# Kernel optimization log

Measured on AMD Instinct MI355X. Metric: run time of the kernel, lower is better.

Reference implementation:

```python
import jax, jax.numpy as jnp
import numpy as np

D = 1024
H = 16
HD = D // H
FF = 4096
B = 2
S = 2048


def _layer_norm(x, g, b, eps=1e-5):
    mu = jnp.mean(x, axis=-1, keepdims=True)
    var = jnp.mean(jnp.square(x - mu), axis=-1, keepdims=True)
    return (x - mu) * jax.lax.rsqrt(var + eps) * g + b


def setup_inputs() -> dict:
    key = jax.random.key(0)
    ks = jax.random.split(key, 16)
    s = 0.02
    return {
        "x": jax.random.normal(ks[0], (B, S, D), jnp.float32),
        "Wq": jax.random.normal(ks[1], (H, D, HD), jnp.float32) * s,
        "bq": jnp.zeros((H, HD), jnp.float32),
        "Wk": jax.random.normal(ks[2], (H, D, HD), jnp.float32) * s,
        "bk": jnp.zeros((H, HD), jnp.float32),
        "Wv": jax.random.normal(ks[3], (H, D, HD), jnp.float32) * s,
        "bv": jnp.zeros((H, HD), jnp.float32),
        "Wo": jax.random.normal(ks[4], (D, D), jnp.float32) * s,
        "bo": jnp.zeros((D,), jnp.float32),
        "W1": jax.random.normal(ks[5], (D, FF), jnp.float32) * s,
        "b1": jnp.zeros((FF,), jnp.float32),
        "W2": jax.random.normal(ks[6], (FF, D), jnp.float32) * s,
        "b2": jnp.zeros((D,), jnp.float32),
        "g1": jnp.ones((D,), jnp.float32),
        "be1": jnp.zeros((D,), jnp.float32),
        "g2": jnp.ones((D,), jnp.float32),
        "be2": jnp.zeros((D,), jnp.float32),
    }


def reference(x, Wq, bq, Wk, bk, Wv, bv, Wo, bo, W1, b1, W2, b2, g1, be1, g2, be2):
    b, s, d = x.shape
    # per-head projections (vectorized over heads)
    q = jnp.einsum("bsd,hde->bhse", x, Wq) + bq[None, :, None, :]
    k = jnp.einsum("bsd,hde->bhse", x, Wk) + bk[None, :, None, :]
    v = jnp.einsum("bsd,hde->bhse", x, Wv) + bv[None, :, None, :]
    # NOTE: source scales by 1/dim_k (not 1/sqrt(dim_k)) -- kept faithful
    scores = jnp.einsum("bhse,bhte->bhst", q, k) / jnp.asarray(HD, x.dtype)
    causal = jnp.tril(jnp.ones((s, s), bool))  # [S,S]
    scores = jnp.where(causal[None, None], scores, jnp.asarray(-jnp.inf, x.dtype))
    attn = jax.nn.softmax(scores, axis=-1)
    ctx = jnp.einsum("bhst,bhte->bhse", attn, v)  # [B,H,S,hd]
    ctx = jnp.transpose(ctx, (0, 2, 1, 3)).reshape(b, s, d)  # concat heads
    attn_out = ctx @ Wo + bo
    x = _layer_norm(x + attn_out, g1, be1)
    # feed-forward: linear -> exact GELU -> linear (dropout = eval identity)
    h = jax.nn.gelu(x @ W1 + b1, approximate=False)
    ff = h @ W2 + b2
    return _layer_norm(x + ff, g2, be2)
```

## Files before the change

kernel.cpp:

```cpp
#include <hip/hip_runtime.h>
#include <math.h>

constexpr int Dm  = 1024;
constexpr int Hh  = 16;
constexpr int HDm = 64;
constexpr int FFm = 4096;
constexpr int Bb  = 2;
constexpr int Sq  = 2048;
constexpr int Mm  = Bb * Sq;

typedef __attribute__((ext_vector_type(8))) short short8;
typedef __attribute__((ext_vector_type(4))) short short4v;
typedef __attribute__((ext_vector_type(4))) float f32x4;

#define AS1 __attribute__((address_space(1)))
#define AS3 __attribute__((address_space(3)))

constexpr float QSCALE = 0.022542110013890054f;

__device__ __forceinline__ unsigned short f2b(float f) {
    union { float f; unsigned u; } v; v.f = f;
    unsigned r = v.u + 0x7FFFu + ((v.u >> 16) & 1u);
    return (unsigned short)(r >> 16);
}

__device__ __forceinline__ float gelu_fast(float x) {
    float z = x * (2.302080918f + 0.102938049f * x * x);
    return x * __builtin_amdgcn_rcpf(1.0f + exp2f(-z));
}

__global__ __launch_bounds__(256) void convert_x(const float* __restrict__ x,
                                                 short* __restrict__ xb) {
    int i = blockIdx.x * 256 + threadIdx.x;
    float4 v = ((const float4*)x)[i];
    short4v o;
    o[0] = (short)f2b(v.x); o[1] = (short)f2b(v.y);
    o[2] = (short)f2b(v.z); o[3] = (short)f2b(v.w);
    ((short4v*)xb)[i] = o;
}

__global__ __launch_bounds__(256) void transpose_to_bf16(
    const float* __restrict__ src, short* __restrict__ dst, int R, int C) {
    __shared__ float t[64][65];
    const int c0 = blockIdx.x * 64, r0 = blockIdx.y * 64;
    const int lc = threadIdx.x & 63, lr4 = threadIdx.x >> 6;
    #pragma unroll
    for (int p = 0; p < 16; ++p) {
        int rr = p * 4 + lr4;
        t[rr][lc] = src[(size_t)(r0 + rr) * C + c0 + lc];
    }
    __syncthreads();
    #pragma unroll
    for (int p = 0; p < 16; ++p) {
        int rr = p * 4 + lr4;
        dst[(size_t)(c0 + rr) * R + r0 + lc] = (short)f2b(t[lc][rr]);
    }
}

__global__ __launch_bounds__(256) void build_wqkv(
    const float* __restrict__ Wq, const float* __restrict__ Wk,
    const float* __restrict__ Wv, short* __restrict__ dst) {
    const int kt = blockIdx.x, h = blockIdx.y, which = blockIdx.z;
    const float* W = ((which == 0) ? Wq : (which == 1) ? Wk : Wv) +
                     (size_t)h * Dm * HDm;
    __shared__ float t[64][65];
    const int lc = threadIdx.x & 63, lr4 = threadIdx.x >> 6;
    #pragma unroll
    for (int p = 0; p < 16; ++p) {
        int kr = p * 4 + lr4;
        t[kr][lc] = W[(size_t)(kt * 64 + kr) * HDm + lc];
    }
    __syncthreads();
    const int nbase = which * 1024 + h * 64;
    #pragma unroll
    for (int p = 0; p < 16; ++p) {
        int e = p * 4 + lr4;
        dst[(size_t)(nbase + e) * Dm + kt * 64 + lc] = (short)f2b(t[lc][e]);
    }
}

__global__ __launch_bounds__(256) void build_bqkv(
    const float* __restrict__ bq, const float* __restrict__ bk,
    const float* __restrict__ bv, float* __restrict__ bcat) {
    int n = blockIdx.x * 256 + threadIdx.x;
    const float* s = (n < 1024) ? bq : (n < 2048) ? bk : bv;
    bcat[n] = s[n & 1023];
}

template<int EPI>
__global__ __launch_bounds__(512, 2) void gemm256(
    const short* __restrict__ A, const short* __restrict__ Bt,
    const float* __restrict__ bias,
    short* __restrict__ outb,
    short* __restrict__ qo, short* __restrict__ ko, short* __restrict__ vo,
    int K, int N, int NMT)
{
    __shared__ __align__(16) char lds[131072];
    char* const ldsA = lds;
    char* const ldsB = lds + 65536;
    const int tid = threadIdx.x;
    const int l = tid & 63, wv = tid >> 6;
    const int wm = wv >> 2, wn = wv & 3;
    const int lr = l & 15, lg = l >> 4;
    const int bid = blockIdx.x;
    const int m0 = (bid % NMT) * 256;
    const int n0 = (bid / NMT) * 256;
    const size_t KB = (size_t)K * 2;
    const int NT = K >> 6;

    const char* pA[2][2];
    const char* pB[2][2];
    #pragma unroll
    for (int i = 0; i < 2; ++i) {
        int c = tid + 512 * i;
        int rh = c >> 3, j = c & 7;
        int sw = (j ^ (rh & 7)) << 4;
        #pragma unroll
        for (int h = 0; h < 2; ++h) {
            pA[h][i] = (const char*)A + (size_t)(m0 + h * 128 + rh) * KB + sw;
            pB[h][i] = (const char*)Bt + (size_t)(n0 + h * 128 + rh) * KB + sw;
        }
    }
    const int dbase = tid * 16;

    f32x4 acc[8][4];
    f32x4 z4 = {0.f, 0.f, 0.f, 0.f};
    #pragma unroll
    for (int i = 0; i < 8; ++i)
        #pragma unroll
        for (int j = 0; j < 4; ++j) acc[i][j] = z4;

#define STAGE_B(h, nb) do {                                                     \
    char* _b = ldsB + ((nb) * 2 + (h)) * 16384;                                 \
    __builtin_amdgcn_global_load_lds((const AS1 void*)pB[h][0],                 \
        (AS3 void*)(_b + dbase), 16, 0, 0);                                     \
    __builtin_amdgcn_global_load_lds((const AS1 void*)pB[h][1],                 \
        (AS3 void*)(_b + dbase + 8192), 16, 0, 0);                              \
    pB[h][0] += 128; pB[h][1] += 128; } while (0)
#define STAGE_A(h, nb) do {                                                     \
    char* _a = ldsA + ((nb) * 2 + (h)) * 16384;                                 \
    __builtin_amdgcn_global_load_lds((const AS1 void*)pA[h][0],                 \
        (AS3 void*)(_a + dbase), 16, 0, 0);                                     \
    __builtin_amdgcn_global_load_lds((const AS1 void*)pA[h][1],                 \
        (AS3 void*)(_a + dbase + 8192), 16, 0, 0);                              \
    pA[h][0] += 128; pA[h][1] += 128; } while (0)

    STAGE_B(0, 0); STAGE_B(1, 0); STAGE_A(0, 0); STAGE_A(1, 0);
    asm volatile("s_waitcnt vmcnt(2)" ::: "memory");
    __builtin_amdgcn_s_barrier();
    __builtin_amdgcn_sched_barrier(0);

    const int swk0 = ((0 + lg) ^ (lr & 7)) << 4;
    const int swk1 = ((4 + lg) ^ (lr & 7)) << 4;

    for (int kt = 0; kt < NT; ++kt) {
        const int buf = kt & 1, nbuf = buf ^ 1;
        const bool more = (kt + 1 < NT);
        char* const Ah0 = ldsA + (buf * 2) * 16384;
        char* const Ah1 = ldsA + (buf * 2 + 1) * 16384;
        char* const Bh  = ldsB + (buf * 2 + (wn >> 1)) * 16384 + (wn & 1) * 8192;

        short8 bf[4][2];
        #pragma unroll
        for (int nf = 0; nf < 4; ++nf) {
            const char* bb = Bh + (nf * 16 + lr) * 128;
            bf[nf][0] = *(const short8*)(bb + swk0);
            bf[nf][1] = *(const short8*)(bb + swk1);
        }
        short8 af[2][2];

#define LOAD_A(p) do {                                                          \
    _Pragma("unroll")                                                           \
    for (int j2 = 0; j2 < 2; ++j2) {                                            \
        const int mf = 2 * (p) + j2;                                            \
        const char* ab = ((mf >> 2) ? Ah1 : Ah0) +                              \
                         ((mf & 3) * 32 + wm * 16 + lr) * 128;                  \
        af[j2][0] = *(const short8*)(ab + swk0);                                \
        af[j2][1] = *(const short8*)(ab + swk1);                                \
    } } while (0)

#define MFMA8(p) do {                                                           \
    _Pragma("unroll")                                                           \
    for (int j2 = 0; j2 < 2; ++j2)                                              \
        _Pragma("unroll")                                                       \
        for (int nf = 0; nf < 4; ++nf) {                                        \
            acc[2 * (p) + j2][nf] = __builtin_amdgcn_mfma_f32_16x16x32_bf16(    \
                af[j2][0], bf[nf][0], acc[2 * (p) + j2][nf], 0, 0, 0);          \
            acc[2 * (p) + j2][nf] = __builtin_amdgcn_mfma_f32_16x16x32_bf16(    \
                af[j2][1], bf[nf][1], acc[2 * (p) + j2][nf], 0, 0, 0);          \
        } } while (0)

        LOAD_A(0);
        if (more) STAGE_B(0, nbuf);
        __builtin_amdgcn_s_barrier();
        asm volatile("s_waitcnt lgkmcnt(0)" ::: "memory");
        __builtin_amdgcn_sched_barrier(0);
        __builtin_amdgcn_s_setprio(1);
        MFMA8(0);
        __builtin_amdgcn_s_setprio(0);
        __builtin_amdgcn_s_barrier();
        LOAD_A(1);
        if (more) STAGE_B(1, nbuf);
        __builtin_amdgcn_s_barrier();
        asm volatile("s_waitcnt lgkmcnt(0)" ::: "memory");
        __builtin_amdgcn_sched_barrier(0);
        __builtin_amdgcn_s_setprio(1);
        MFMA8(1);
        __builtin_amdgcn_s_setprio(0);
        if (more) asm volatile("s_waitcnt vmcnt(4)" ::: "memory");
        else      asm volatile("s_waitcnt vmcnt(0)" ::: "memory");
        __builtin_amdgcn_s_barrier();
        __builtin_amdgcn_sched_barrier(0);
        LOAD_A(2);
        if (more) STAGE_A(0, nbuf);
        __builtin_amdgcn_s_barrier();
        asm volatile("s_waitcnt lgkmcnt(0)" ::: "memory");
        __builtin_amdgcn_sched_barrier(0);
        __builtin_amdgcn_s_setprio(1);
        MFMA8(2);
        __builtin_amdgcn_s_setprio(0);
        __builtin_amdgcn_s_barrier();
        LOAD_A(3);
        if (more) STAGE_A(1, nbuf);
        __builtin_amdgcn_s_barrier();
        asm volatile("s_waitcnt lgkmcnt(0)" ::: "memory");
        __builtin_amdgcn_sched_barrier(0);
        __builtin_amdgcn_s_setprio(1);
        MFMA8(3);
        __builtin_amdgcn_s_setprio(0);
        asm volatile("s_waitcnt vmcnt(2)" ::: "memory");
        __builtin_amdgcn_s_barrier();
        __builtin_amdgcn_sched_barrier(0);
#undef LOAD_A
#undef MFMA8
    }

    #pragma unroll
    for (int mf = 0; mf < 8; ++mf) {
        #pragma unroll
        for (int nf = 0; nf < 4; ++nf) {
            const int n = n0 + wn * 64 + nf * 16 + lr;
            const int mB = m0 + mf * 32 + wm * 16 + lg * 4;
            if (EPI == 1) {
                #pragma unroll
                for (int r = 0; r < 4; ++r) {
                    float val = gelu_fast(acc[mf][nf][r] + bias[n]);
                    outb[(size_t)(mB + r) * N + n] = (short)f2b(val);
                }
            } else {
                const int which = n >> 10, hh = (n >> 6) & 15, e = n & 63;
                const int bb2 = mB >> 11, ss = mB & 2047;
                if (which == 2) {
                    short4v pk;
                    #pragma unroll
                    for (int r = 0; r < 4; ++r)
                        pk[r] = (short)f2b(acc[mf][nf][r] + bias[n]);
                    *(short4v*)&vo[(((size_t)bb2 * Hh + hh) * HDm + e) * Sq + ss] = pk;
                } else {
                    short* o = (which == 0) ? qo : ko;
                    const float sc = (which == 0) ? QSCALE : 1.0f;
                    #pragma unroll
                    for (int r = 0; r < 4; ++r) {
                        float val = (acc[mf][nf][r] + bias[n]) * sc;
                        o[(((size_t)bb2 * Hh + hh) * Sq + ss + r) * HDm + e] = (short)f2b(val);
                    }
                }
            }
        }
    }
#undef STAGE_A
#undef STAGE_B
}

template<int EPI, int BM>
__global__ __launch_bounds__(256, 2) void gemm128dp(
    const short* __restrict__ A, const short* __restrict__ Bt,
    const float* __restrict__ bias, const float* __restrict__ res,
    float* __restrict__ outf, short* __restrict__ outb,
    int K, int N)
{
    constexpr int AR  = BM / 32;
    constexpr int BMW = BM / 2;
    constexpr int MF  = BMW / 16;
    constexpr int ABUF = BM * 128;
    __shared__ __align__(16) char lds[2 * ABUF + 32768];
    char* const ldsA = lds;
    char* const ldsB = lds + 2 * ABUF;
    const int tid = threadIdx.x;
    const int l = tid & 63, wv = tid >> 6;
    const int wr = wv >> 1, wc = wv & 1;
    const int lr = l & 15, lg = l >> 4;
    const int m0 = blockIdx.x * BM, n0 = blockIdx.y * 128;
    const size_t KB = (size_t)K * 2;
    const int NT = K >> 6;

    const int r0 = tid >> 3, jj = tid & 7;
    const int sw = (jj ^ (r0 & 7)) << 4;
    const char* aSrc[AR]; const char* bSrc1[2]; const char* bSrc2[2];
    #pragma unroll
    for (int i = 0; i < AR; ++i)
        aSrc[i] = (const char*)A + (size_t)(m0 + r0 + 32 * i) * KB + sw;
    #pragma unroll
    for (int i = 0; i < 2; ++i) {
        bSrc1[i] = (const char*)Bt + (size_t)(n0 + r0 + 64 * i) * KB + sw;
        bSrc2[i] = (const char*)Bt + (size_t)(n0 + 32 + r0 + 64 * i) * KB + sw;
    }
    const int aDst0 = tid * 16;

#define STAGE_SA(nb) do {                                                       \
    char* _a = ldsA + (nb) * ABUF;                                              \
    _Pragma("unroll")                                                           \
    for (int i = 0; i < AR; ++i) {                                              \
        __builtin_amdgcn_global_load_lds((const AS1 void*)aSrc[i],              \
            (AS3 void*)(_a + aDst0 + i * 4096), 16, 0, 0);                      \
        aSrc[i] += 128;                                                         \
    } } while (0)
#define STAGE_SB1(nb) do {                                                      \
    char* _b = ldsB + (nb) * 16384;                                             \
    _Pragma("unroll")                                                           \
    for (int i = 0; i < 2; ++i) {                                               \
        __builtin_amdgcn_global_load_lds((const AS1 void*)bSrc1[i],             \
            (AS3 void*)(_b + aDst0 + i * 8192), 16, 0, 0);                      \
        bSrc1[i] += 128;                                                        \
    } } while (0)
#define STAGE_SB2(nb) do {                                                      \
    char* _b = ldsB + (nb) * 16384 + 4096;                                      \
    _Pragma("unroll")                                                           \
    for (int i = 0; i < 2; ++i) {                                               \
        __builtin_amdgcn_global_load_lds((const AS1 void*)bSrc2[i],             \
            (AS3 void*)(_b + aDst0 + i * 8192), 16, 0, 0);                      \
        bSrc2[i] += 128;                                                        \
    } } while (0)

    f32x4 acc[MF][4];
    f32x4 z4 = {0.f, 0.f, 0.f, 0.f};
    #pragma unroll
    for (int i = 0; i < MF; ++i)
        #pragma unroll
        for (int j = 0; j < 4; ++j) acc[i][j] = z4;

    STAGE_SA(0); STAGE_SB1(0); STAGE_SB2(0);
    asm volatile("s_waitcnt vmcnt(2)" ::: "memory");
    __builtin_amdgcn_s_barrier();
    __builtin_amdgcn_sched_barrier(0);

    for (int kt = 0; kt < NT; ++kt) {
        const int buf = kt & 1, nbuf = buf ^ 1;
        const bool more = (kt + 1 < NT);
        char* const Ab = ldsA + buf * ABUF;
        char* const Bb = ldsB + buf * 16384;

        short8 af[MF][2], bf[2][2];
        #pragma unroll
        for (int mf = 0; mf < MF; ++mf) {
            const int row = wr * BMW + mf * 16 + lr;
            const char* ab = Ab + row * 128;
            af[mf][0] = *(const short8*)(ab + (((0 + lg) ^ (row & 7)) << 4));
            af[mf][1] = *(const short8*)(ab + (((4 + lg) ^ (row & 7)) << 4));
        }
        #pragma unroll
        for (int nf = 0; nf < 2; ++nf) {
            const int row = wc * 64 + nf * 16 + lr;
            const char* bb = Bb + row * 128;
            bf[nf][0] = *(const short8*)(bb + (((0 + lg) ^ (row & 7)) << 4));
            bf[nf][1] = *(const short8*)(bb + (((4 + lg) ^ (row & 7)) << 4));
        }
        if (more) STAGE_SA(nbuf);
        asm volatile("s_waitcnt lgkmcnt(0)" ::: "memory");
        __builtin_amdgcn_sched_barrier(0);
        __builtin_amdgcn_s_setprio(1);
        #pragma unroll
        for (int mf = 0; mf < MF; ++mf)
            #pragma unroll
            for (int nf = 0; nf < 2; ++nf) {
                acc[mf][nf] = __builtin_amdgcn_mfma_f32_16x16x32_bf16(
                    af[mf][0], bf[nf][0], acc[mf][nf], 0, 0, 0);
                acc[mf][nf] = __builtin_amdgcn_mfma_f32_16x16x32_bf16(
                    af[mf][1], bf[nf][1], acc[mf][nf], 0, 0, 0);
            }
        __builtin_amdgcn_s_setprio(0);
        if (more) {
            if constexpr (BM == 128) asm volatile("s_waitcnt vmcnt(4)" ::: "memory");
            else                     asm volatile("s_waitcnt vmcnt(2)" ::: "memory");
        } else {
            asm volatile("s_waitcnt vmcnt(0)" ::: "memory");
        }
        __builtin_amdgcn_s_barrier();
        __builtin_amdgcn_sched_barrier(0);

        #pragma unroll
        for (int nf = 0; nf < 2; ++nf) {
            const int row = wc * 64 + (nf + 2) * 16 + lr;
            const char* bb = Bb + row * 128;
            bf[nf][0] = *(const short8*)(bb + (((0 + lg) ^ (row & 7)) << 4));
            bf[nf][1] = *(const short8*)(bb + (((4 + lg) ^ (row & 7)) << 4));
        }
        if (more) { STAGE_SB1(nbuf); STAGE_SB2(nbuf); }
        asm volatile("s_waitcnt lgkmcnt(0)" ::: "memory");
        __builtin_amdgcn_sched_barrier(0);
        __builtin_amdgcn_s_setprio(1);
        #pragma unroll
        for (int mf = 0; mf < MF; ++mf)
            #pragma unroll
            for (int nf = 0; nf < 2; ++nf) {
                acc[mf][nf + 2] = __builtin_amdgcn_mfma_f32_16x16x32_bf16(
                    af[mf][0], bf[nf][0], acc[mf][nf + 2], 0, 0, 0);
                acc[mf][nf + 2] = __builtin_amdgcn_mfma_f32_16x16x32_bf16(
                    af[mf][1], bf[nf][1], acc[mf][nf + 2], 0, 0, 0);
            }
        __builtin_amdgcn_s_setprio(0);
        if (more) {
            asm volatile("s_waitcnt vmcnt(2)" ::: "memory");
            __builtin_amdgcn_s_barrier();
            __builtin_amdgcn_sched_barrier(0);
        }
    }

    #pragma unroll
    for (int mf = 0; mf < MF; ++mf) {
        #pragma unroll
        for (int nf = 0; nf < 4; ++nf) {
            #pragma unroll
            for (int r = 0; r < 4; ++r) {
                int m = m0 + wr * BMW + mf * 16 + lg * 4 + r;
                int n = n0 + wc * 64 + nf * 16 + lr;
                float val = acc[mf][nf][r];
                if (EPI == 0) {
                    val += bias[n] + res[(size_t)m * N + n];
                    outf[(size_t)m * N + n] = val;
                } else {
                    val = gelu_fast(val + bias[n]);
                    outb[(size_t)m * N + n] = (short)f2b(val);
                }
            }
        }
    }
#undef STAGE_SA
#undef STAGE_SB1
#undef STAGE_SB2
}

__global__ __launch_bounds__(256) void attn_mfma(
    const short* __restrict__ qg, const short* __restrict__ kg,
    const short* __restrict__ vtg, short* __restrict__ ctx)
{
    const int bid = blockIdx.x;
    const int qt = (Sq / 64 - 1) - (bid >> 5);
    const int hb = bid & 31;
    const int h = hb & 15, b = hb >> 4;
    const int tid = threadIdx.x;
    const int l = tid & 63, wv = tid >> 6;
    const int lr = l & 15, lg = l >> 4;

    __shared__ __align__(16) char KlB[8192];
    __shared__ __align__(16) char VtB[8192];
    __shared__ __align__(16) char PlB[4][2048];

    const size_t bh = ((size_t)b * Hh + h) * Sq;
    const size_t vbase = ((size_t)b * Hh + h) * HDm * Sq;

    const int qbase = qt * 64 + wv * 16;
    short8 aq[2];
    #pragma unroll
    for (int ks = 0; ks < 2; ++ks)
        aq[ks] = *(const short8*)(qg + (bh + qbase + lr) * HDm + ks * 32 + lg * 8);

    f32x4 zero4 = {0.f, 0.f, 0.f, 0.f};
    f32x4 oacc[4], lacc = zero4;
    #pragma unroll
    for (int i = 0; i < 4; ++i) oacc[i] = zero4;
    float mreg[4];
    #pragma unroll
    for (int r = 0; r < 4; ++r) mreg[r] = -3e38f;

    short8 vone;
    #pragma unroll
    for (int j = 0; j < 8; ++j) vone[j] = (short)0x3F80;

    char* plw = PlB[wv];

    const char* srcK[2]; const char* srcV[2];
    #pragma unroll
    for (int r2 = 0; r2 < 2; ++r2) {
        int cl = tid + 256 * r2;
        int row = cl >> 3, j = cl & 7;
        srcK[r2] = (const char*)kg + ((bh + row) * HDm + ((j ^ (row & 7)) * 8)) * 2;
        srcV[r2] = (const char*)vtg + (vbase + (size_t)row * Sq + ((j ^ (row & 7)) * 8)) * 2;
    }

    const int nt = qt + 1;
    for (int tk = 0; tk < nt; ++tk) {
        __syncthreads();
        #pragma unroll
        for (int r2 = 0; r2 < 2; ++r2) {
            int c = tid + 256 * r2;
            __builtin_amdgcn_global_load_lds((const AS1 void*)srcK[r2],
                (AS3 void*)(KlB + c * 16), 16, 0, 0);
            srcK[r2] += 64 * HDm * 2;
            __builtin_amdgcn_global_load_lds((const AS1 void*)srcV[r2],
                (AS3 void*)(VtB + c * 16), 16, 0, 0);
            srcV[r2] += 64 * 2;
        }
        __syncthreads();

        f32x4 sc[4];
        #pragma unroll
        for (int i = 0; i < 4; ++i) sc[i] = zero4;
        __builtin_amdgcn_s_setprio(1);
        #pragma unroll
        for (int kd = 0; kd < 2; ++kd) {
            #pragma unroll
            for (int nf = 0; nf < 4; ++nf) {
                short8 bk = *(const short8*)(KlB + (nf * 16 + lr) * 128 +
                                (((kd * 4 + lg) ^ (lr & 7)) << 4));
                sc[nf] = __builtin_amdgcn_mfma_f32_16x16x32_bf16(
                    aq[kd], bk, sc[nf], 0, 0, 0);
            }
        }
        __builtin_amdgcn_s_setprio(0);

        if (tk == qt) {
            #pragma unroll
            for (int r = 0; r < 4; ++r) {
                const int qglob = qbase + lg * 4 + r;
                #pragma unroll
                for (int nf = 0; nf < 4; ++nf)
                    if (tk * 64 + nf * 16 + lr > qglob) sc[nf][r] = -3e38f;
            }
        }

        float lm[4];
        #pragma unroll
        for (int r = 0; r < 4; ++r)
            lm[r] = fmaxf(fmaxf(sc[0][r], sc[1][r]), fmaxf(sc[2][r], sc[3][r]));
        bool grow = (lm[0] > mreg[0] + 8.f) || (lm[1] > mreg[1] + 8.f) ||
                    (lm[2] > mreg[2] + 8.f) || (lm[3] > mreg[3] + 8.f);

        if (__any((int)grow)) {
            #pragma unroll
            for (int r = 0; r < 4; ++r) {
                float mr = lm[r];
                #pragma unroll
                for (int o = 1; o < 16; o <<= 1)
                    mr = fmaxf(mr, __shfl_xor(mr, o));
                float mnew = fmaxf(mreg[r], mr);
                float cf = exp2f(mreg[r] - mnew);
                mreg[r] = mnew;
                const int prow = lg * 4 + r;
                #pragma unroll
                for (int nf = 0; nf < 4; ++nf) {
                    float p = exp2f(sc[nf][r] - mnew);
                    *(unsigned short*)(plw + prow * 128 +
                        (((nf * 2 + (lr >> 3)) ^ (prow & 7)) << 4) +
                        ((lr & 7) << 1)) = (unsigned short)(__float_as_uint(p) >> 16);
                }
                #pragma unroll
                for (int nf = 0; nf < 4; ++nf) oacc[nf][r] *= cf;
                lacc[r] *= cf;
            }
        } else {
            #pragma unroll
            for (int r = 0; r < 4; ++r) {
                const int prow = lg * 4 + r;
                #pragma unroll
                for (int nf = 0; nf < 4; ++nf) {
                    float p = exp2f(sc[nf][r] - mreg[r]);
                    *(unsigned short*)(plw + prow * 128 +
                        (((nf * 2 + (lr >> 3)) ^ (prow & 7)) << 4) +
                        ((lr & 7) << 1)) = (unsigned short)(__float_as_uint(p) >> 16);
                }
            }
        }

        asm volatile("s_waitcnt lgkmcnt(0)" ::: "memory");
        __builtin_amdgcn_sched_barrier(0);

        __builtin_amdgcn_s_setprio(1);
        #pragma unroll
        for (int ks = 0; ks < 2; ++ks) {
            short8 pa = *(const short8*)(plw + lr * 128 +
                            (((ks * 4 + lg) ^ (lr & 7)) << 4));
            #pragma unroll
            for (int nf = 0; nf < 4; ++nf) {
                short8 bv8 = *(const short8*)(VtB + (nf * 16 + lr) * 128 +
                                (((ks * 4 + lg) ^ (lr & 7)) << 4));
                oacc[nf] = __builtin_amdgcn_mfma_f32_16x16x32_bf16(
                    pa, bv8, oacc[nf], 0, 0, 0);
            }
            lacc = __builtin_amdgcn_mfma_f32_16x16x32_bf16(pa, vone, lacc, 0, 0, 0);
        }
        __builtin_amdgcn_s_setprio(0);
    }

    #pragma unroll
    for (int r = 0; r < 4; ++r) {
        float inv = 1.0f / lacc[r];
        int q = qbase + lg * 4 + r;
        size_t o = ((size_t)b * Sq + q) * Dm + h * HDm;
        #pragma unroll
        for (int nf = 0; nf < 4; ++nf)
            ctx[o + nf * 16 + lr] = (short)f2b(oacc[nf][r] * inv);
    }
}

template<int BF16OUT>
__global__ __launch_bounds__(256) void ln_kernel(
    const float* __restrict__ in, const float* __restrict__ g,
    const float* __restrict__ be, float* __restrict__ outf,
    short* __restrict__ outb)
{
    const int m = blockIdx.x;
    const int tid = threadIdx.x;
    const float4 vl = *(const float4*)&in[(size_t)m * Dm + tid * 4];
    float s  = vl.x + vl.y + vl.z + vl.w;
    float s2 = vl.x * vl.x + vl.y * vl.y + vl.z * vl.z + vl.w * vl.w;
    #pragma unroll
    for (int o = 32; o > 0; o >>= 1) {
        s  += __shfl_down(s, o);
        s2 += __shfl_down(s2, o);
    }
    __shared__ float rs[4], rs2[4];
    const int w = tid >> 6;
    if ((tid & 63) == 0) { rs[w] = s; rs2[w] = s2; }
    __syncthreads();
    s  = rs[0] + rs[1] + rs[2] + rs[3];
    s2 = rs2[0] + rs2[1] + rs2[2] + rs2[3];
    const float mean = s * (1.0f / Dm);
    const float var  = s2 * (1.0f / Dm) - mean * mean;
    const float rstd = rsqrtf(var + 1e-5f);
    const float4 gv = *(const float4*)&g[tid * 4];
    const float4 bv = *(const float4*)&be[tid * 4];
    float4 ov;
    ov.x = (vl.x - mean) * rstd * gv.x + bv.x;
    ov.y = (vl.y - mean) * rstd * gv.y + bv.y;
    ov.z = (vl.z - mean) * rstd * gv.z + bv.z;
    ov.w = (vl.w - mean) * rstd * gv.w + bv.w;
    *(float4*)&outf[(size_t)m * Dm + tid * 4] = ov;
    if (BF16OUT) {
        short4v o4;
        o4[0] = (short)f2b(ov.x); o4[1] = (short)f2b(ov.y);
        o4[2] = (short)f2b(ov.z); o4[3] = (short)f2b(ov.w);
        *(short4v*)&outb[(size_t)m * Dm + tid * 4] = o4;
    }
}

extern "C" void kernel_launch(void* const* d_in, const int* in_sizes, int n_in,
                              void* d_out, int out_size, void* d_ws, size_t ws_size,
                              hipStream_t stream)
{
    const float* x  = (const float*)d_in[0];
    const float* Wq = (const float*)d_in[1];
    const float* bq = (const float*)d_in[2];
    const float* Wk = (const float*)d_in[3];
    const float* bk = (const float*)d_in[4];
    const float* Wv = (const float*)d_in[5];
    const float* bv = (const float*)d_in[6];
    const float* Wo = (const float*)d_in[7];
    const float* bo = (const float*)d_in[8];
    const float* W1 = (const float*)d_in[9];
    const float* b1 = (const float*)d_in[10];
    const float* W2 = (const float*)d_in[11];
    const float* b2 = (const float*)d_in[12];
    const float* g1 = (const float*)d_in[13];
    const float* be1= (const float*)d_in[14];
    const float* g2 = (const float*)d_in[15];
    const float* be2= (const float*)d_in[16];
    float* out = (float*)d_out;

    char* ws = (char*)d_ws;
    size_t off = 0;
    auto alloc = [&](size_t bytes) {
        char* p = ws + off;
        off += (bytes + 255) & ~(size_t)255;
        return p;
    };
    const size_t MD2 = (size_t)Mm * Dm * 2;
    short* xb    = (short*)alloc(MD2);
    short* wqkvt = (short*)alloc((size_t)3072 * Dm * 2);
    float* bcat  = (float*)alloc(3072 * 4);
    short* wot   = (short*)alloc((size_t)Dm * Dm * 2);
    short* w1t   = (short*)alloc((size_t)FFm * Dm * 2);
    short* w2t   = (short*)alloc((size_t)Dm * FFm * 2);
    short* qb    = (short*)alloc(MD2);
    short* kb    = (short*)alloc(MD2);
    short* vtb   = (short*)alloc(MD2);
    short* ctxb  = (short*)alloc(MD2);
    short* hb    = qb;
    float* y     = (float*)alloc((size_t)Mm * Dm * 4);
    float* x1f   = (float*)alloc((size_t)Mm * Dm * 4);
    short* x1b   = (short*)alloc(MD2);
    float* y2    = y;

    convert_x<<<Mm * Dm / 1024, 256, 0, stream>>>(x, xb);
    build_wqkv<<<dim3(16, 16, 3), 256, 0, stream>>>(Wq, Wk, Wv, wqkvt);
    build_bqkv<<<12, 256, 0, stream>>>(bq, bk, bv, bcat);
    transpose_to_bf16<<<dim3(16, 16), 256, 0, stream>>>(Wo, wot, Dm, Dm);
    transpose_to_bf16<<<dim3(64, 16), 256, 0, stream>>>(W1, w1t, Dm, FFm);
    transpose_to_bf16<<<dim3(16, 64), 256, 0, stream>>>(W2, w2t, FFm, Dm);

    gemm256<2><<<192, 512, 0, stream>>>(
        xb, wqkvt, bcat, nullptr, qb, kb, vtb, Dm, 3072, 16);
    attn_mfma<<<1024, 256, 0, stream>>>(qb, kb, vtb, ctxb);
    gemm128dp<0, 64><<<dim3(64, 8), 256, 0, stream>>>(
        ctxb, wot, bo, x, y, nullptr, Dm, Dm);
    ln_kernel<1><<<Mm, 256, 0, stream>>>(y, g1, be1, x1f, x1b);
    gemm256<1><<<256, 512, 0, stream>>>(
        x1b, w1t, b1, hb, nullptr, nullptr, nullptr, Dm, FFm, 16);
    gemm128dp<0, 64><<<dim3(64, 8), 256, 0, stream>>>(
        hb, w2t, b2, x1f, y2, nullptr, FFm, Dm);
    ln_kernel<0><<<Mm, 256, 0, stream>>>(y2, g2, be2, out, nullptr);
}
```

Measured before the change: 235.5 us.

## Enlarge attention query tiles to 128 rows and drop fp32 LN1 copy

The attention kernel now runs 512-thread blocks covering 128 query rows, so each K/V tile loaded into LDS serves eight waves instead of four. The block-to-(head, q-tile) mapping is reordered to pair heavy and light causal tiles, and waves skip K tiles that lie entirely above their causal limit. Separately, the first LayerNorm writes only a bf16 output, and the second projection GEMM reads its residual from that bf16 copy, removing an fp32 write and read. The residual is now held at bf16 precision, which adds rounding error to the output; the causal skip can leave waves idle while they still take part in the block barriers.

```diff
diff --git a/kernel.cpp b/kernel.cpp
--- a/kernel.cpp
+++ b/kernel.cpp
@@ -22,6 +22,10 @@
     union { float f; unsigned u; } v; v.f = f;
     unsigned r = v.u + 0x7FFFu + ((v.u >> 16) & 1u);
     return (unsigned short)(r >> 16);
+}
+__device__ __forceinline__ float b2f(unsigned short s) {
+    union { unsigned u; float f; } v; v.u = ((unsigned)s) << 16;
+    return v.f;
 }
 
 __device__ __forceinline__ float gelu_fast(float x) {
@@ -276,7 +280,8 @@
 __global__ __launch_bounds__(256, 2) void gemm128dp(
     const short* __restrict__ A, const short* __restrict__ Bt,
     const float* __restrict__ bias, const float* __restrict__ res,
-    float* __restrict__ outf, short* __restrict__ outb,
+    const short* __restrict__ resb,
+    float* __restrict__ outf,
     int K, int N)
 {
     constexpr int AR  = BM / 32;
@@ -424,14 +429,10 @@
             for (int r = 0; r < 4; ++r) {
                 int m = m0 + wr * BMW + mf * 16 + lg * 4 + r;
                 int n = n0 + wc * 64 + nf * 16 + lr;
-                float val = acc[mf][nf][r];
-                if (EPI == 0) {
-                    val += bias[n] + res[(size_t)m * N + n];
-                    outf[(size_t)m * N + n] = val;
-                } else {
-                    val = gelu_fast(val + bias[n]);
-                    outb[(size_t)m * N + n] = (short)f2b(val);
-                }
+                float val = acc[mf][nf][r] + bias[n];
+                if (EPI == 0) val += res[(size_t)m * N + n];
+                else          val += b2f(((const unsigned short*)resb)[(size_t)m * N + n]);
+                outf[(size_t)m * N + n] = val;
             }
         }
     }
@@ -440,13 +441,14 @@
 #undef STAGE_SB2
 }
 
-__global__ __launch_bounds__(256) void attn_mfma(
+__global__ __launch_bounds__(512) void attn_mfma(
     const short* __restrict__ qg, const short* __restrict__ kg,
     const short* __restrict__ vtg, short* __restrict__ ctx)
 {
     const int bid = blockIdx.x;
-    const int qt = (Sq / 64 - 1) - (bid >> 5);
-    const int hb = bid & 31;
+    int qt, hb;
+    if (bid < 256) { hb = bid >> 4;              qt = 15 - (bid & 15); }
+    else           { hb = ((bid >> 4) & 15) + 16; qt = bid & 15; }
     const int h = hb & 15, b = hb >> 4;
     const int tid = threadIdx.x;
     const int l = tid & 63, wv = tid >> 6;
@@ -454,12 +456,12 @@
 
     __shared__ __align__(16) char KlB[8192];
     __shared__ __align__(16) char VtB[8192];
-    __shared__ __align__(16) char PlB[4][2048];
+    __shared__ __align__(16) char PlB[8][2048];
 
     const size_t bh = ((size_t)b * Hh + h) * Sq;
     const size_t vbase = ((size_t)b * Hh + h) * HDm * Sq;
 
-    const int qbase = qt * 64 + wv * 16;
+    const int qbase = qt * 128 + wv * 16;
     short8 aq[2];
     #pragma unroll
     for (int ks = 0; ks < 2; ++ks)
@@ -479,29 +481,25 @@
 
     char* plw = PlB[wv];
 
-    const char* srcK[2]; const char* srcV[2];
-    #pragma unroll
-    for (int r2 = 0; r2 < 2; ++r2) {
-        int cl = tid + 256 * r2;
-        int row = cl >> 3, j = cl & 7;
-        srcK[r2] = (const char*)kg + ((bh + row) * HDm + ((j ^ (row & 7)) * 8)) * 2;
-        srcV[r2] = (const char*)vtg + (vbase + (size_t)row * Sq + ((j ^ (row & 7)) * 8)) * 2;
-    }
-
-    const int nt = qt + 1;
+    const int srow = tid >> 3, sj = tid & 7;
+    const char* srcK = (const char*)kg +
+        ((bh + srow) * HDm + ((sj ^ (srow & 7)) * 8)) * 2;
+    const char* srcV = (const char*)vtg +
+        (vbase + (size_t)srow * Sq + ((sj ^ (srow & 7)) * 8)) * 2;
+    const int sdst = tid * 16;
+
+    const int nt = 2 * qt + 2;
     for (int tk = 0; tk < nt; ++tk) {
         __syncthreads();
-        #pragma unroll
-        for (int r2 = 0; r2 < 2; ++r2) {
-            int c = tid + 256 * r2;
-            __builtin_amdgcn_global_load_lds((const AS1 void*)srcK[r2],
-                (AS3 void*)(KlB + c * 16), 16, 0, 0);
-            srcK[r2] += 64 * HDm * 2;
-            __builtin_amdgcn_global_load_lds((const AS1 void*)srcV[r2],
-                (AS3 void*)(VtB + c * 16), 16, 0, 0);
-            srcV[r2] += 64 * 2;
-        }
+        __builtin_amdgcn_global_load_lds((const AS1 void*)srcK,
+            (AS3 void*)(KlB + sdst), 16, 0, 0);
+        srcK += 64 * HDm * 2;
+        __builtin_amdgcn_global_load_lds((const AS1 void*)srcV,
+            (AS3 void*)(VtB + sdst), 16, 0, 0);
+        srcV += 64 * 2;
         __syncthreads();
+
+        if (tk * 64 > qbase + 15) continue;
 
         f32x4 sc[4];
         #pragma unroll
@@ -519,7 +517,7 @@
         }
         __builtin_amdgcn_s_setprio(0);
 
-        if (tk == qt) {
+        if (tk * 64 + 63 > qbase) {
             #pragma unroll
             for (int r = 0; r < 4; ++r) {
                 const int qglob = qbase + lg * 4 + r;
@@ -603,7 +601,7 @@
     }
 }
 
-template<int BF16OUT>
+template<int MODE>
 __global__ __launch_bounds__(256) void ln_kernel(
     const float* __restrict__ in, const float* __restrict__ g,
     const float* __restrict__ be, float* __restrict__ outf,
@@ -635,8 +633,9 @@
     ov.y = (vl.y - mean) * rstd * gv.y + bv.y;
     ov.z = (vl.z - mean) * rstd * gv.z + bv.z;
     ov.w = (vl.w - mean) * rstd * gv.w + bv.w;
-    *(float4*)&outf[(size_t)m * Dm + tid * 4] = ov;
-    if (BF16OUT) {
+    if (MODE == 0) {
+        *(float4*)&outf[(size_t)m * Dm + tid * 4] = ov;
+    } else {
         short4v o4;
         o4[0] = (short)f2b(ov.x); o4[1] = (short)f2b(ov.y);
         o4[2] = (short)f2b(ov.z); o4[3] = (short)f2b(ov.w);
@@ -687,7 +686,6 @@
     short* ctxb  = (short*)alloc(MD2);
     short* hb    = qb;
     float* y     = (float*)alloc((size_t)Mm * Dm * 4);
-    float* x1f   = (float*)alloc((size_t)Mm * Dm * 4);
     short* x1b   = (short*)alloc(MD2);
     float* y2    = y;
 
@@ -700,13 +698,13 @@
 
     gemm256<2><<<192, 512, 0, stream>>>(
         xb, wqkvt, bcat, nullptr, qb, kb, vtb, Dm, 3072, 16);
-    attn_mfma<<<1024, 256, 0, stream>>>(qb, kb, vtb, ctxb);
+    attn_mfma<<<512, 512, 0, stream>>>(qb, kb, vtb, ctxb);
     gemm128dp<0, 64><<<dim3(64, 8), 256, 0, stream>>>(
-        ctxb, wot, bo, x, y, nullptr, Dm, Dm);
-    ln_kernel<1><<<Mm, 256, 0, stream>>>(y, g1, be1, x1f, x1b);
+        ctxb, wot, bo, x, nullptr, y, Dm, Dm);
+    ln_kernel<1><<<Mm, 256, 0, stream>>>(y, g1, be1, nullptr, x1b);
     gemm256<1><<<256, 512, 0, stream>>>(
         x1b, w1t, b1, hb, nullptr, nullptr, nullptr, Dm, FFm, 16);
-    gemm128dp<0, 64><<<dim3(64, 8), 256, 0, stream>>>(
-        hb, w2t, b2, x1f, y2, nullptr, FFm, Dm);
+    gemm128dp<2, 64><<<dim3(64, 8), 256, 0, stream>>>(
+        hb, w2t, b2, nullptr, x1b, y2, FFm, Dm);
     ln_kernel<0><<<Mm, 256, 0, stream>>>(y2, g2, be2, out, nullptr);
 }
```

Result: no change. 233.3 us (-0.9%).

## Merge prep kernels, transpose MFMA outputs for vector epilogues, use bf16 residual

Applied to the files above, without the earlier changes.

Folds the six weight/input preparation launches into one kernel that dispatches on block index. Swaps the A/B operands of the MFMA calls so each lane holds four consecutive columns, which lets the bias loads and output stores use 4-wide vectors; the V-transpose store becomes four scalar stores instead. The first LayerNorm now writes only bf16, and the second FFN GEMM reads its residual from that bf16 copy, removing an fp32 write and read. Using the bf16 residual adds rounding error to the skip connection.

```diff
diff --git a/kernel.cpp b/kernel.cpp
--- a/kernel.cpp
+++ b/kernel.cpp
@@ -23,27 +23,22 @@
     unsigned r = v.u + 0x7FFFu + ((v.u >> 16) & 1u);
     return (unsigned short)(r >> 16);
 }
+__device__ __forceinline__ float b2f(unsigned short s) {
+    union { unsigned u; float f; } v; v.u = ((unsigned)s) << 16;
+    return v.f;
+}
 
 __device__ __forceinline__ float gelu_fast(float x) {
     float z = x * (2.302080918f + 0.102938049f * x * x);
     return x * __builtin_amdgcn_rcpf(1.0f + exp2f(-z));
 }
 
-__global__ __launch_bounds__(256) void convert_x(const float* __restrict__ x,
-                                                 short* __restrict__ xb) {
-    int i = blockIdx.x * 256 + threadIdx.x;
-    float4 v = ((const float4*)x)[i];
-    short4v o;
-    o[0] = (short)f2b(v.x); o[1] = (short)f2b(v.y);
-    o[2] = (short)f2b(v.z); o[3] = (short)f2b(v.w);
-    ((short4v*)xb)[i] = o;
-}
-
-__global__ __launch_bounds__(256) void transpose_to_bf16(
-    const float* __restrict__ src, short* __restrict__ dst, int R, int C) {
-    __shared__ float t[64][65];
-    const int c0 = blockIdx.x * 64, r0 = blockIdx.y * 64;
-    const int lc = threadIdx.x & 63, lr4 = threadIdx.x >> 6;
+__device__ __forceinline__ void transpose_body(
+    const float* __restrict__ src, short* __restrict__ dst,
+    int R, int C, int bx, int by, int tid, float (*t)[65])
+{
+    const int c0 = bx * 64, r0 = by * 64;
+    const int lc = tid & 63, lr4 = tid >> 6;
     #pragma unroll
     for (int p = 0; p < 16; ++p) {
         int rr = p * 4 + lr4;
@@ -57,34 +52,56 @@
     }
 }
 
-__global__ __launch_bounds__(256) void build_wqkv(
+__global__ __launch_bounds__(256) void prep_all(
+    const float* __restrict__ x,  short* __restrict__ xb,
     const float* __restrict__ Wq, const float* __restrict__ Wk,
-    const float* __restrict__ Wv, short* __restrict__ dst) {
-    const int kt = blockIdx.x, h = blockIdx.y, which = blockIdx.z;
-    const float* W = ((which == 0) ? Wq : (which == 1) ? Wk : Wv) +
-                     (size_t)h * Dm * HDm;
+    const float* __restrict__ Wv, short* __restrict__ wqkvt,
+    const float* __restrict__ bq, const float* __restrict__ bk,
+    const float* __restrict__ bv, float* __restrict__ bcat,
+    const float* __restrict__ Wo, short* __restrict__ wot,
+    const float* __restrict__ W1, short* __restrict__ w1t,
+    const float* __restrict__ W2, short* __restrict__ w2t)
+{
     __shared__ float t[64][65];
-    const int lc = threadIdx.x & 63, lr4 = threadIdx.x >> 6;
-    #pragma unroll
-    for (int p = 0; p < 16; ++p) {
-        int kr = p * 4 + lr4;
-        t[kr][lc] = W[(size_t)(kt * 64 + kr) * HDm + lc];
-    }
-    __syncthreads();
-    const int nbase = which * 1024 + h * 64;
-    #pragma unroll
-    for (int p = 0; p < 16; ++p) {
-        int e = p * 4 + lr4;
-        dst[(size_t)(nbase + e) * Dm + kt * 64 + lc] = (short)f2b(t[lc][e]);
-    }
-}
-
-__global__ __launch_bounds__(256) void build_bqkv(
-    const float* __restrict__ bq, const float* __restrict__ bk,
-    const float* __restrict__ bv, float* __restrict__ bcat) {
-    int n = blockIdx.x * 256 + threadIdx.x;
-    const float* s = (n < 1024) ? bq : (n < 2048) ? bk : bv;
-    bcat[n] = s[n & 1023];
+    const int bid = blockIdx.x, tid = threadIdx.x;
+    if (bid < 256) {
+        transpose_body(Wo, wot, Dm, Dm, bid & 15, bid >> 4, tid, t);
+    } else if (bid < 1280) {
+        int lo = bid - 256;
+        transpose_body(W1, w1t, Dm, FFm, lo & 63, lo >> 6, tid, t);
+    } else if (bid < 2304) {
+        int lo = bid - 1280;
+        transpose_body(W2, w2t, FFm, Dm, lo & 15, lo >> 4, tid, t);
+    } else if (bid < 2316) {
+        int n = (bid - 2304) * 256 + tid;
+        const float* s = (n < 1024) ? bq : (n < 2048) ? bk : bv;
+        bcat[n] = s[n & 1023];
+    } else if (bid < 3084) {
+        int lo = bid - 2316;
+        const int kt = lo & 15, h = (lo >> 4) & 15, which = lo >> 8;
+        const float* W = ((which == 0) ? Wq : (which == 1) ? Wk : Wv) +
+                         (size_t)h * Dm * HDm;
+        const int lc = tid & 63, lr4 = tid >> 6;
+        #pragma unroll
+        for (int p = 0; p < 16; ++p) {
+            int kr = p * 4 + lr4;
+            t[kr][lc] = W[(size_t)(kt * 64 + kr) * HDm + lc];
+        }
+        __syncthreads();
+        const int nbase = which * 1024 + h * 64;
+        #pragma unroll
+        for (int p = 0; p < 16; ++p) {
+            int e = p * 4 + lr4;
+            wqkvt[(size_t)(nbase + e) * Dm + kt * 64 + lc] = (short)f2b(t[lc][e]);
+        }
+    } else {
+        int i = (bid - 3084) * 256 + tid;
+        float4 v = ((const float4*)x)[i];
+        short4v o;
+        o[0] = (short)f2b(v.x); o[1] = (short)f2b(v.y);
+        o[2] = (short)f2b(v.z); o[3] = (short)f2b(v.w);
+        ((short4v*)xb)[i] = o;
+    }
 }
 
 template<int EPI>
@@ -185,9 +202,9 @@
         _Pragma("unroll")                                                       \
         for (int nf = 0; nf < 4; ++nf) {                                        \
             acc[2 * (p) + j2][nf] = __builtin_amdgcn_mfma_f32_16x16x32_bf16(    \
-                af[j2][0], bf[nf][0], acc[2 * (p) + j2][nf], 0, 0, 0);          \
+                bf[nf][0], af[j2][0], acc[2 * (p) + j2][nf], 0, 0, 0);          \
             acc[2 * (p) + j2][nf] = __builtin_amdgcn_mfma_f32_16x16x32_bf16(    \
-                af[j2][1], bf[nf][1], acc[2 * (p) + j2][nf], 0, 0, 0);          \
+                bf[nf][1], af[j2][1], acc[2 * (p) + j2][nf], 0, 0, 0);          \
         } } while (0)
 
         LOAD_A(0);
@@ -239,31 +256,38 @@
     for (int mf = 0; mf < 8; ++mf) {
         #pragma unroll
         for (int nf = 0; nf < 4; ++nf) {
-            const int n = n0 + wn * 64 + nf * 16 + lr;
-            const int mB = m0 + mf * 32 + wm * 16 + lg * 4;
+            const int m  = m0 + mf * 32 + wm * 16 + lr;
+            const int nb = n0 + wn * 64 + nf * 16 + lg * 4;
+            const float4 b4 = *(const float4*)&bias[nb];
+            float v0 = acc[mf][nf][0] + b4.x;
+            float v1 = acc[mf][nf][1] + b4.y;
+            float v2 = acc[mf][nf][2] + b4.z;
+            float v3 = acc[mf][nf][3] + b4.w;
             if (EPI == 1) {
-                #pragma unroll
-                for (int r = 0; r < 4; ++r) {
-                    float val = gelu_fast(acc[mf][nf][r] + bias[n]);
-                    outb[(size_t)(mB + r) * N + n] = (short)f2b(val);
-                }
+                short4v pk;
+                pk[0] = (short)f2b(gelu_fast(v0));
+                pk[1] = (short)f2b(gelu_fast(v1));
+                pk[2] = (short)f2b(gelu_fast(v2));
+                pk[3] = (short)f2b(gelu_fast(v3));
+                *(short4v*)&outb[(size_t)m * N + nb] = pk;
             } else {
-                const int which = n >> 10, hh = (n >> 6) & 15, e = n & 63;
-                const int bb2 = mB >> 11, ss = mB & 2047;
+                const int which = nb >> 10, hh = (nb >> 6) & 15, e0 = nb & 63;
+                const int bb2 = m >> 11, ss = m & 2047;
                 if (which == 2) {
-                    short4v pk;
-                    #pragma unroll
-                    for (int r = 0; r < 4; ++r)
-                        pk[r] = (short)f2b(acc[mf][nf][r] + bias[n]);
-                    *(short4v*)&vo[(((size_t)bb2 * Hh + hh) * HDm + e) * Sq + ss] = pk;
+                    size_t base = (((size_t)bb2 * Hh + hh) * HDm + e0) * Sq + ss;
+                    vo[base]          = (short)f2b(v0);
+                    vo[base + Sq]     = (short)f2b(v1);
+                    vo[base + 2 * Sq] = (short)f2b(v2);
+                    vo[base + 3 * Sq] = (short)f2b(v3);
                 } else {
                     short* o = (which == 0) ? qo : ko;
                     const float sc = (which == 0) ? QSCALE : 1.0f;
-                    #pragma unroll
-                    for (int r = 0; r < 4; ++r) {
-                        float val = (acc[mf][nf][r] + bias[n]) * sc;
-                        o[(((size_t)bb2 * Hh + hh) * Sq + ss + r) * HDm + e] = (short)f2b(val);
-                    }
+                    short4v pk;
+                    pk[0] = (short)f2b(v0 * sc);
+                    pk[1] = (short)f2b(v1 * sc);
+                    pk[2] = (short)f2b(v2 * sc);
+                    pk[3] = (short)f2b(v3 * sc);
+                    *(short4v*)&o[(((size_t)bb2 * Hh + hh) * Sq + ss) * HDm + e0] = pk;
                 }
             }
         }
@@ -276,7 +300,8 @@
 __global__ __launch_bounds__(256, 2) void gemm128dp(
     const short* __restrict__ A, const short* __restrict__ Bt,
     const float* __restrict__ bias, const float* __restrict__ res,
-    float* __restrict__ outf, short* __restrict__ outb,
+    const short* __restrict__ resb,
+    float* __restrict__ outf,
     int K, int N)
 {
     constexpr int AR  = BM / 32;
@@ -374,9 +399,9 @@
             #pragma unroll
             for (int nf = 0; nf < 2; ++nf) {
                 acc[mf][nf] = __builtin_amdgcn_mfma_f32_16x16x32_bf16(
-                    af[mf][0], bf[nf][0], acc[mf][nf], 0, 0, 0);
+                    bf[nf][0], af[mf][0], acc[mf][nf], 0, 0, 0);
                 acc[mf][nf] = __builtin_amdgcn_mfma_f32_16x16x32_bf16(
-                    af[mf][1], bf[nf][1], acc[mf][nf], 0, 0, 0);
+                    bf[nf][1], af[mf][1], acc[mf][nf], 0, 0, 0);
             }
         __builtin_amdgcn_s_setprio(0);
         if (more) {
@@ -404,9 +429,9 @@
             #pragma unroll
             for (int nf = 0; nf < 2; ++nf) {
                 acc[mf][nf + 2] = __builtin_amdgcn_mfma_f32_16x16x32_bf16(
-                    af[mf][0], bf[nf][0], acc[mf][nf + 2], 0, 0, 0);
+                    bf[nf][0], af[mf][0], acc[mf][nf + 2], 0, 0, 0);
                 acc[mf][nf + 2] = __builtin_amdgcn_mfma_f32_16x16x32_bf16(
-                    af[mf][1], bf[nf][1], acc[mf][nf + 2], 0, 0, 0);
+                    bf[nf][1], af[mf][1], acc[mf][nf + 2], 0, 0, 0);
             }
         __builtin_amdgcn_s_setprio(0);
         if (more) {
@@ -420,19 +445,25 @@
     for (int mf = 0; mf < MF; ++mf) {
         #pragma unroll
         for (int nf = 0; nf < 4; ++nf) {
-            #pragma unroll
-            for (int r = 0; r < 4; ++r) {
-                int m = m0 + wr * BMW + mf * 16 + lg * 4 + r;
-                int n = n0 + wc * 64 + nf * 16 + lr;
-                float val = acc[mf][nf][r];
-                if (EPI == 0) {
-                    val += bias[n] + res[(size_t)m * N + n];
-                    outf[(size_t)m * N + n] = val;
-                } else {
-                    val = gelu_fast(val + bias[n]);
-                    outb[(size_t)m * N + n] = (short)f2b(val);
-                }
-            }
+            const int m  = m0 + wr * BMW + mf * 16 + lr;
+            const int nb = n0 + wc * 64 + nf * 16 + lg * 4;
+            const float4 b4 = *(const float4*)&bias[nb];
+            float4 o4;
+            o4.x = acc[mf][nf][0] + b4.x;
+            o4.y = acc[mf][nf][1] + b4.y;
+            o4.z = acc[mf][nf][2] + b4.z;
+            o4.w = acc[mf][nf][3] + b4.w;
+            if (EPI == 0) {
+                const float4 r4 = *(const float4*)&res[(size_t)m * N + nb];
+                o4.x += r4.x; o4.y += r4.y; o4.z += r4.z; o4.w += r4.w;
+            } else {
+                const short4v r4 = *(const short4v*)&resb[(size_t)m * N + nb];
+                o4.x += b2f((unsigned short)r4[0]);
+                o4.y += b2f((unsigned short)r4[1]);
+                o4.z += b2f((unsigned short)r4[2]);
+                o4.w += b2f((unsigned short)r4[3]);
+            }
+            *(float4*)&outf[(size_t)m * N + nb] = o4;
         }
     }
 #undef STAGE_SA
@@ -603,7 +634,7 @@
     }
 }
 
-template<int BF16OUT>
+template<int MODE>
 __global__ __launch_bounds__(256) void ln_kernel(
     const float* __restrict__ in, const float* __restrict__ g,
     const float* __restrict__ be, float* __restrict__ outf,
@@ -635,8 +666,9 @@
     ov.y = (vl.y - mean) * rstd * gv.y + bv.y;
     ov.z = (vl.z - mean) * rstd * gv.z + bv.z;
     ov.w = (vl.w - mean) * rstd * gv.w + bv.w;
-    *(float4*)&outf[(size_t)m * Dm + tid * 4] = ov;
-    if (BF16OUT) {
+    if (MODE == 0) {
+        *(float4*)&outf[(size_t)m * Dm + tid * 4] = ov;
+    } else {
         short4v o4;
         o4[0] = (short)f2b(ov.x); o4[1] = (short)f2b(ov.y);
         o4[2] = (short)f2b(ov.z); o4[3] = (short)f2b(ov.w);
@@ -687,26 +719,22 @@
     short* ctxb  = (short*)alloc(MD2);
     short* hb    = qb;
     float* y     = (float*)alloc((size_t)Mm * Dm * 4);
-    float* x1f   = (float*)alloc((size_t)Mm * Dm * 4);
     short* x1b   = (short*)alloc(MD2);
     float* y2    = y;
 
-    convert_x<<<Mm * Dm / 1024, 256, 0, stream>>>(x, xb);
-    build_wqkv<<<dim3(16, 16, 3), 256, 0, stream>>>(Wq, Wk, Wv, wqkvt);
-    build_bqkv<<<12, 256, 0, stream>>>(bq, bk, bv, bcat);
-    transpose_to_bf16<<<dim3(16, 16), 256, 0, stream>>>(Wo, wot, Dm, Dm);
-    transpose_to_bf16<<<dim3(64, 16), 256, 0, stream>>>(W1, w1t, Dm, FFm);
-    transpose_to_bf16<<<dim3(16, 64), 256, 0, stream>>>(W2, w2t, FFm, Dm);
+    prep_all<<<7180, 256, 0, stream>>>(
+        x, xb, Wq, Wk, Wv, wqkvt, bq, bk, bv, bcat,
+        Wo, wot, W1, w1t, W2, w2t);
 
     gemm256<2><<<192, 512, 0, stream>>>(
         xb, wqkvt, bcat, nullptr, qb, kb, vtb, Dm, 3072, 16);
     attn_mfma<<<1024, 256, 0, stream>>>(qb, kb, vtb, ctxb);
     gemm128dp<0, 64><<<dim3(64, 8), 256, 0, stream>>>(
-        ctxb, wot, bo, x, y, nullptr, Dm, Dm);
-    ln_kernel<1><<<Mm, 256, 0, stream>>>(y, g1, be1, x1f, x1b);
+        ctxb, wot, bo, x, nullptr, y, Dm, Dm);
+    ln_kernel<1><<<Mm, 256, 0, stream>>>(y, g1, be1, nullptr, x1b);
     gemm256<1><<<256, 512, 0, stream>>>(
         x1b, w1t, b1, hb, nullptr, nullptr, nullptr, Dm, FFm, 16);
-    gemm128dp<0, 64><<<dim3(64, 8), 256, 0, stream>>>(
-        hb, w2t, b2, x1f, y2, nullptr, FFm, Dm);
+    gemm128dp<2, 64><<<dim3(64, 8), 256, 0, stream>>>(
+        hb, w2t, b2, nullptr, x1b, y2, FFm, Dm);
     ln_kernel<0><<<Mm, 256, 0, stream>>>(y2, g2, be2, out, nullptr);
 }
```

Result: faster. 226.7 us (-3.8%).
